# Kernel optimization log

Hardware: AMD Instinct MI355X
Metric: run time of the kernel (lower is better)

The kernel has to match this reference:

```python
import jax, jax.numpy as jnp
import numpy as np

EPS = 0.1  # eps added to covariance sums, as in torch cov()
N, D, N_CLASSES = 4096, 1024, 64


def setup_inputs() -> dict:
    key = jax.random.key(0)
    k1, k2 = jax.random.split(key)
    inputs = jax.random.normal(k1, (N, D), dtype=jnp.float32)
    targets = jax.random.randint(k2, (N,), 0, N_CLASSES, dtype=jnp.int32)
    return {"inputs": inputs, "targets": targets}


def _masked_sqdiff_sum(M, x):
    # Per-dim sum over masked pairs (i,j) of (x_i - x_j)^2, without
    # materializing the [n, n, d] difference tensor:
    #   sum_ij M_ij (x_id^2 + x_jd^2 - 2 x_id x_jd)
    row = M.sum(axis=1)  # [n]
    col = M.sum(axis=0)  # [n]
    x2 = x * x
    return row @ x2 + col @ x2 - 2.0 * jnp.sum(x * (M @ x), axis=0)  # [d]


def _jeffrey_loss(inputs, targets):
    n = inputs.shape[0]
    same = targets[:, None] == targets[None, :]
    eye = jnp.eye(n, dtype=bool)
    pos_m = (same & ~eye).astype(inputs.dtype)  # positive pairs, i != j
    neg_m = (~same).astype(inputs.dtype)        # negative pairs

    # Covariances are computed on detached diffs in the torch code
    xd = jax.lax.stop_gradient(inputs)
    cnt_pos = pos_m.sum()
    cnt_neg = neg_m.sum()
    sigma1 = (_masked_sqdiff_sum(pos_m, xd) + EPS) / cnt_pos  # [d]
    sigma0 = (_masked_sqdiff_sum(neg_m, xd) + EPS) / cnt_neg  # [d]
    weights = 1.0 / sigma0 - 1.0 / sigma1  # [d], constant w.r.t. grad

    # S[i, j] = sum_d weights_d * (x_i - x_j)_d^2, via gram expansion
    xw = inputs * weights            # [n, d]
    sq = jnp.sum(inputs * xw, axis=1)  # [n], sum_d w_d x_d^2
    S = sq[:, None] + sq[None, :] - 2.0 * inputs @ xw.T  # [n, n]

    # BCEWithLogitsLoss(mean): label 1 on positive pairs (logits a),
    # label 0 on negative pairs (logits b)
    loss_sum = jnp.sum(pos_m * jax.nn.softplus(-S)) + jnp.sum(neg_m * jax.nn.softplus(S))
    return loss_sum / (cnt_pos + cnt_neg)


def reference(inputs, targets):
    return _jeffrey_loss(inputs, targets)
```

## Files before the change

kernel.cpp:

```cpp
#include <hip/hip_runtime.h>
#include <stdint.h>

#define N_ROWS 4096
#define DIM    1024
#define NCLS   64
#define EPSV   0.1f

typedef __attribute__((ext_vector_type(8))) __bf16 bf16x8;
typedef __attribute__((ext_vector_type(4))) float  f32x4;

__device__ __forceinline__ unsigned short f2bf(float f) {
    union { float f; unsigned u; } v; v.f = f;
    unsigned r = v.u + 0x7FFF + ((v.u >> 16) & 1);
    return (unsigned short)(r >> 16);
}

__device__ __forceinline__ void async_cp16(const void* g, void* l) {
    __builtin_amdgcn_global_load_lds((const __attribute__((address_space(1))) void*)g,
                                     (__attribute__((address_space(3))) void*)l,
                                     16, 0, 0);
}

__device__ __forceinline__ float softplus(float x) {
    return fmaxf(x, 0.f) + __logf(1.f + __expf(-fabsf(x)));
}

__global__ __launch_bounds__(128) void k_stats(const float* __restrict__ X,
                                               const int* __restrict__ tgt,
                                               float* __restrict__ csum_p,
                                               float* __restrict__ csq_p) {
    __shared__ float csum[NCLS * 128];
    __shared__ float csq[NCLS * 128];
    __shared__ int   tch[128];
    int tid = threadIdx.x;
    int dg = blockIdx.x >> 5, ch = blockIdx.x & 31;
    int d = dg * 128 + tid;
    for (int c = 0; c < NCLS; c++) { csum[c * 128 + tid] = 0.f; csq[c * 128 + tid] = 0.f; }
    tch[tid] = tgt[ch * 128 + tid];
    __syncthreads();
    const float* xp = X + (size_t)(ch * 128) * DIM + d;
    #pragma unroll 4
    for (int r = 0; r < 128; r++) {
        float x = xp[(size_t)r * DIM];
        int t = tch[r];
        csum[t * 128 + tid] += x;
        csq [t * 128 + tid] += x * x;
    }
    for (int c = 0; c < NCLS; c++) {
        csum_p[(size_t)(ch * NCLS + c) * DIM + d] = csum[c * 128 + tid];
        csq_p [(size_t)(ch * NCLS + c) * DIM + d] = csq [c * 128 + tid];
    }
}

__global__ __launch_bounds__(256) void k_reduce(const float* __restrict__ csum_p,
                                                const float* __restrict__ csq_p,
                                                float* __restrict__ csumR,
                                                float* __restrict__ csqR) {
    int idx = blockIdx.x * 256 + threadIdx.x;
    float s = 0.f, q = 0.f;
    #pragma unroll 8
    for (int ch = 0; ch < 32; ch++) {
        s += csum_p[(size_t)ch * NCLS * DIM + idx];
        q += csq_p [(size_t)ch * NCLS * DIM + idx];
    }
    csumR[idx] = s;
    csqR [idx] = q;
}

__global__ __launch_bounds__(256) void k_weights(const int* __restrict__ tgt,
                                                 const float* __restrict__ csumR,
                                                 const float* __restrict__ csqR,
                                                 float* __restrict__ w,
                                                 float* __restrict__ loss_out) {
    __shared__ int hist[NCLS];
    int tid = threadIdx.x;
    if (tid < NCLS) hist[tid] = 0;
    __syncthreads();
    for (int i = tid; i < N_ROWS; i += 256) atomicAdd(&hist[tgt[i]], 1);
    __syncthreads();
    float cnt_pos, cnt_neg;
    {
        long long sp = 0, ss = 0;
        for (int c = 0; c < NCLS; c++) { long long cc = hist[c]; sp += cc * (cc - 1); ss += cc * cc; }
        cnt_pos = (float)sp;
        cnt_neg = (float)((long long)N_ROWS * N_ROWS - ss);
    }
    int d = blockIdx.x * 256 + tid;
    float A = 0.f, X2 = 0.f, T = 0.f, SS = 0.f;
    #pragma unroll 8
    for (int c = 0; c < NCLS; c++) {
        float s = csumR[c * DIM + d];
        float q = csqR [c * DIM + d];
        A += (float)hist[c] * q; X2 += q; T += s; SS += s * s;
    }
    float posnum = 2.f * (A - SS);
    float negnum = 2.f * ((float)N_ROWS * X2 - A - T * T + SS);
    w[d] = cnt_neg / (negnum + EPSV) - cnt_pos / (posnum + EPSV);
    if (blockIdx.x == 0 && tid == 0) loss_out[0] = 0.0f;
}

__global__ __launch_bounds__(256) void k_prep(const float* __restrict__ X,
                                              const float* __restrict__ w,
                                              unsigned short* __restrict__ Xb,
                                              unsigned short* __restrict__ XWb,
                                              float* __restrict__ sq) {
    int row = blockIdx.x, tid = threadIdx.x;
    const float4* xr = (const float4*)(X + (size_t)row * DIM);
    const float4* wr = (const float4*)w;
    float4 x = xr[tid], ww = wr[tid];
    float4 xw = make_float4(x.x * ww.x, x.y * ww.y, x.z * ww.z, x.w * ww.w);
    float p = x.x * xw.x + x.y * xw.y + x.z * xw.z + x.w * xw.w;
    ushort4 xb, xwb;
    xb.x  = f2bf(x.x);  xb.y  = f2bf(x.y);  xb.z  = f2bf(x.z);  xb.w  = f2bf(x.w);
    xwb.x = f2bf(xw.x); xwb.y = f2bf(xw.y); xwb.z = f2bf(xw.z); xwb.w = f2bf(xw.w);
    ((ushort4*)(Xb  + (size_t)row * DIM))[tid] = xb;
    ((ushort4*)(XWb + (size_t)row * DIM))[tid] = xwb;
    for (int off = 32; off; off >>= 1) p += __shfl_down(p, off, 64);
    __shared__ float red[4];
    int wv = tid >> 6, ln = tid & 63;
    if (ln == 0) red[wv] = p;
    __syncthreads();
    if (tid == 0) sq[row] = red[0] + red[1] + red[2] + red[3];
}

__global__ __launch_bounds__(512) void k_gemm_loss(const unsigned short* __restrict__ Xb,
                                                   const unsigned short* __restrict__ XWb,
                                                   const float* __restrict__ sq,
                                                   const int* __restrict__ tgt,
                                                   float* __restrict__ loss) {
    __shared__ __align__(16) unsigned short As[3][128 * 32];
    __shared__ __align__(16) unsigned short Bs[3][128 * 32];
    __shared__ float sqI[128], sqJ[128];
    __shared__ int   tIs[128], tJs[128];
    __shared__ float red[8];

    int tid = threadIdx.x;
    int wave = tid >> 6, lane = tid & 63;

    int g = blockIdx.x & 7, s = blockIdx.x >> 3;
    int sz0 = g + 1, sz1 = g + 9, sz2 = g + 17, sz3 = g + 25;
    int jt, it;
    if      (s < sz0)             { jt = g;      it = s; }
    else if (s < sz0 + sz1)       { jt = g + 8;  it = s - sz0; }
    else if (s < sz0 + sz1 + sz2) { jt = g + 16; it = s - sz0 - sz1; }
    else if (s < sz0 + sz1 + sz2 + sz3) { jt = g + 24; it = s - sz0 - sz1 - sz2; }
    else return;

    const unsigned short* gp[2];
    unsigned short* lb[2];
    #pragma unroll
    for (int si = 0; si < 2; si++) {
        int gI = wave * 2 + si;
        int R  = gI * 16 + (lane >> 2);
        int q  = (lane & 3) ^ ((R >> 1) & 3);
        int r  = R & 127;
        bool isA = R < 128;
        int grow = (isA ? it : jt) * 128 + r;
        const unsigned short* src = isA ? Xb : XWb;
        gp[si] = src + (size_t)grow * DIM + q * 8;
        lb[si] = (isA ? &As[0][0] : &Bs[0][0]) + (gI & 7) * (16 * 32);
    }

    int lr = lane & 15, kq = lane >> 4;
    int offA[4], offB[2];
    int wrow = (wave >> 2) * 64, wcol = (wave & 3) * 32;
    #pragma unroll
    for (int mi = 0; mi < 4; mi++) {
        int row = wrow + mi * 16 + lr;
        offA[mi] = row * 32 + (kq ^ ((row >> 1) & 3)) * 8;
    }
    #pragma unroll
    for (int nj = 0; nj < 2; nj++) {
        int col = wcol + nj * 16 + lr;
        offB[nj] = col * 32 + (kq ^ ((col >> 1) & 3)) * 8;
    }

    f32x4 acc[4][2];
    #pragma unroll
    for (int i = 0; i < 4; i++)
        #pragma unroll
        for (int j = 0; j < 2; j++) acc[i][j] = (f32x4){0.f, 0.f, 0.f, 0.f};

    #pragma unroll
    for (int si = 0; si < 2; si++) async_cp16(gp[si], lb[si]);
    #pragma unroll
    for (int si = 0; si < 2; si++) async_cp16(gp[si] + 32, lb[si] + 128 * 32);

    int rd = 0;
    for (int kk = 0; kk < 32; kk++) {
        if (kk != 31) asm volatile("s_waitcnt vmcnt(2)" ::: "memory");
        else          asm volatile("s_waitcnt vmcnt(0)" ::: "memory");
        asm volatile("s_barrier" ::: "memory");
        if (kk < 30) {
            int wr = rd ? rd - 1 : 2;
            #pragma unroll
            for (int si = 0; si < 2; si++)
                async_cp16(gp[si] + (kk + 2) * 32, lb[si] + wr * (128 * 32));
        }
        const unsigned short* Ab = As[rd];
        const unsigned short* Bb = Bs[rd];
        bf16x8 av[4], bv[2];
        #pragma unroll
        for (int i = 0; i < 4; i++) av[i] = *(const bf16x8*)(Ab + offA[i]);
        #pragma unroll
        for (int j = 0; j < 2; j++) bv[j] = *(const bf16x8*)(Bb + offB[j]);
        #pragma unroll
        for (int i = 0; i < 4; i++)
            #pragma unroll
            for (int j = 0; j < 2; j++)
                acc[i][j] = __builtin_amdgcn_mfma_f32_16x16x32_bf16(av[i], bv[j], acc[i][j], 0, 0, 0);
        rd = (rd == 2) ? 0 : rd + 1;
    }

    __syncthreads();
    if (tid < 128)      { sqI[tid] = sq[it * 128 + tid]; tIs[tid] = tgt[it * 128 + tid]; }
    else if (tid < 256) { int u = tid - 128; sqJ[u] = sq[jt * 128 + u]; tJs[u] = tgt[jt * 128 + u]; }
    __syncthreads();

    float sum = 0.f;
    bool diagTile = (it == jt);
    #pragma unroll
    for (int j = 0; j < 2; j++) {
        int col = wcol + j * 16 + (lane & 15);
        float sj = sqJ[col]; int tj = tJs[col];
        #pragma unroll
        for (int i = 0; i < 4; i++) {
            int rbase = wrow + i * 16 + (lane >> 4) * 4;
            #pragma unroll
            for (int r = 0; r < 4; r++) {
                int rowp = rbase + r;
                float S = sqI[rowp] + sj - 2.f * acc[i][j][r];
                float v;
                if (tIs[rowp] == tj) v = (diagTile && rowp == col) ? 0.f : softplus(-S);
                else                 v = softplus(S);
                sum += v;
            }
        }
    }
    float scale = (diagTile ? 1.f : 2.f) * (1.f / ((float)N_ROWS * (float)(N_ROWS - 1)));
    sum *= scale;
    for (int off = 32; off; off >>= 1) sum += __shfl_down(sum, off, 64);
    if (lane == 0) red[wave] = sum;
    __syncthreads();
    if (tid == 0) {
        float t = 0.f;
        #pragma unroll
        for (int wv = 0; wv < 8; wv++) t += red[wv];
        atomicAdd(loss, t);
    }
}

extern "C" void kernel_launch(void* const* d_in, const int* in_sizes, int n_in,
                              void* d_out, int out_size, void* d_ws, size_t ws_size,
                              hipStream_t stream) {
    const float* X  = (const float*)d_in[0];
    const int* tgt  = (const int*)d_in[1];
    float* out = (float*)d_out;
    char* ws = (char*)d_ws;
    const size_t MB = 1u << 20;

    float* w        = (float*)ws;
    float* sq       = (float*)(ws + 4096);
    unsigned short* Xb  = (unsigned short*)(ws + 1 * MB);
    unsigned short* XWb = (unsigned short*)(ws + 9 * MB);
    float* csum_p   = (float*)(ws + 17 * MB);
    float* csq_p    = (float*)(ws + 25 * MB);
    float* csumR    = (float*)(ws + 33 * MB);
    float* csqR     = (float*)(ws + 33 * MB + 256 * 1024);

    k_stats   <<<256,  128, 0, stream>>>(X, tgt, csum_p, csq_p);
    k_reduce  <<<256,  256, 0, stream>>>(csum_p, csq_p, csumR, csqR);
    k_weights <<<4,    256, 0, stream>>>(tgt, csumR, csqR, w, out);
    k_prep    <<<4096, 256, 0, stream>>>(X, w, Xb, XWb, sq);
    k_gemm_loss<<<640, 512, 0, stream>>>(Xb, XWb, sq, tgt, out);
}
```

Baseline: 136.2 us.

## Fuse per-class stats into one gather kernel and deepen GEMM pipeline to four stages

Replaces the two-kernel per-class statistics pass with a single kernel. Each block compacts the row indices of its class into shared memory, then accumulates the sum and sum of squares directly, which removes the 16 MB of partial-sum writes and the separate reduction launch. Separately, the GEMM's LDS ring grows from three to four stages so three k-tiles are in flight instead of two. The trade-off is more LDS per block, which may reduce occupancy, and an index-gathered read of X where each row is still read contiguously.

```diff
diff --git a/kernel.cpp b/kernel.cpp
--- a/kernel.cpp
+++ b/kernel.cpp
@@ -25,46 +25,29 @@
     return fmaxf(x, 0.f) + __logf(1.f + __expf(-fabsf(x)));
 }
 
-__global__ __launch_bounds__(128) void k_stats(const float* __restrict__ X,
-                                               const int* __restrict__ tgt,
-                                               float* __restrict__ csum_p,
-                                               float* __restrict__ csq_p) {
-    __shared__ float csum[NCLS * 128];
-    __shared__ float csq[NCLS * 128];
-    __shared__ int   tch[128];
-    int tid = threadIdx.x;
-    int dg = blockIdx.x >> 5, ch = blockIdx.x & 31;
-    int d = dg * 128 + tid;
-    for (int c = 0; c < NCLS; c++) { csum[c * 128 + tid] = 0.f; csq[c * 128 + tid] = 0.f; }
-    tch[tid] = tgt[ch * 128 + tid];
-    __syncthreads();
-    const float* xp = X + (size_t)(ch * 128) * DIM + d;
-    #pragma unroll 4
-    for (int r = 0; r < 128; r++) {
-        float x = xp[(size_t)r * DIM];
-        int t = tch[r];
-        csum[t * 128 + tid] += x;
-        csq [t * 128 + tid] += x * x;
-    }
-    for (int c = 0; c < NCLS; c++) {
-        csum_p[(size_t)(ch * NCLS + c) * DIM + d] = csum[c * 128 + tid];
-        csq_p [(size_t)(ch * NCLS + c) * DIM + d] = csq [c * 128 + tid];
-    }
-}
-
-__global__ __launch_bounds__(256) void k_reduce(const float* __restrict__ csum_p,
-                                                const float* __restrict__ csq_p,
+__global__ __launch_bounds__(256) void k_cstats(const float* __restrict__ X,
+                                                const int* __restrict__ tgt,
                                                 float* __restrict__ csumR,
                                                 float* __restrict__ csqR) {
-    int idx = blockIdx.x * 256 + threadIdx.x;
-    float s = 0.f, q = 0.f;
-    #pragma unroll 8
-    for (int ch = 0; ch < 32; ch++) {
-        s += csum_p[(size_t)ch * NCLS * DIM + idx];
-        q += csq_p [(size_t)ch * NCLS * DIM + idx];
-    }
-    csumR[idx] = s;
-    csqR [idx] = q;
+    __shared__ int rows[N_ROWS];
+    __shared__ int nrows_s;
+    int tid = threadIdx.x;
+    int c = blockIdx.x >> 2, q = blockIdx.x & 3;
+    if (tid == 0) nrows_s = 0;
+    __syncthreads();
+    for (int i = tid; i < N_ROWS; i += 256)
+        if (tgt[i] == c) { int p = atomicAdd(&nrows_s, 1); rows[p] = i; }
+    __syncthreads();
+    int n = nrows_s;
+    int d = q * 256 + tid;
+    float s = 0.f, qq = 0.f;
+    #pragma unroll 4
+    for (int r = 0; r < n; r++) {
+        float x = X[(size_t)rows[r] * DIM + d];
+        s += x; qq += x * x;
+    }
+    csumR[c * DIM + d] = s;
+    csqR [c * DIM + d] = qq;
 }
 
 __global__ __launch_bounds__(256) void k_weights(const int* __restrict__ tgt,
@@ -128,8 +111,8 @@
                                                    const float* __restrict__ sq,
                                                    const int* __restrict__ tgt,
                                                    float* __restrict__ loss) {
-    __shared__ __align__(16) unsigned short As[3][128 * 32];
-    __shared__ __align__(16) unsigned short Bs[3][128 * 32];
+    __shared__ __align__(16) unsigned short As[4][128 * 32];
+    __shared__ __align__(16) unsigned short Bs[4][128 * 32];
     __shared__ float sqI[128], sqJ[128];
     __shared__ int   tIs[128], tJs[128];
     __shared__ float red[8];
@@ -182,21 +165,23 @@
         for (int j = 0; j < 2; j++) acc[i][j] = (f32x4){0.f, 0.f, 0.f, 0.f};
 
     #pragma unroll
-    for (int si = 0; si < 2; si++) async_cp16(gp[si], lb[si]);
-    #pragma unroll
-    for (int si = 0; si < 2; si++) async_cp16(gp[si] + 32, lb[si] + 128 * 32);
-
-    int rd = 0;
+    for (int st = 0; st < 3; st++)
+        #pragma unroll
+        for (int si = 0; si < 2; si++)
+            async_cp16(gp[si] + st * 32, lb[si] + st * (128 * 32));
+
     for (int kk = 0; kk < 32; kk++) {
-        if (kk != 31) asm volatile("s_waitcnt vmcnt(2)" ::: "memory");
-        else          asm volatile("s_waitcnt vmcnt(0)" ::: "memory");
+        if      (kk < 30)  asm volatile("s_waitcnt vmcnt(4)" ::: "memory");
+        else if (kk == 30) asm volatile("s_waitcnt vmcnt(2)" ::: "memory");
+        else               asm volatile("s_waitcnt vmcnt(0)" ::: "memory");
         asm volatile("s_barrier" ::: "memory");
-        if (kk < 30) {
-            int wr = rd ? rd - 1 : 2;
+        if (kk < 29) {
+            int wr = (kk + 3) & 3;
             #pragma unroll
             for (int si = 0; si < 2; si++)
-                async_cp16(gp[si] + (kk + 2) * 32, lb[si] + wr * (128 * 32));
+                async_cp16(gp[si] + (kk + 3) * 32, lb[si] + wr * (128 * 32));
         }
+        int rd = kk & 3;
         const unsigned short* Ab = As[rd];
         const unsigned short* Bb = Bs[rd];
         bf16x8 av[4], bv[2];
@@ -209,7 +194,6 @@
             #pragma unroll
             for (int j = 0; j < 2; j++)
                 acc[i][j] = __builtin_amdgcn_mfma_f32_16x16x32_bf16(av[i], bv[j], acc[i][j], 0, 0, 0);
-        rd = (rd == 2) ? 0 : rd + 1;
     }
 
     __syncthreads();
@@ -263,13 +247,10 @@
     float* sq       = (float*)(ws + 4096);
     unsigned short* Xb  = (unsigned short*)(ws + 1 * MB);
     unsigned short* XWb = (unsigned short*)(ws + 9 * MB);
-    float* csum_p   = (float*)(ws + 17 * MB);
-    float* csq_p    = (float*)(ws + 25 * MB);
-    float* csumR    = (float*)(ws + 33 * MB);
-    float* csqR     = (float*)(ws + 33 * MB + 256 * 1024);
-
-    k_stats   <<<256,  128, 0, stream>>>(X, tgt, csum_p, csq_p);
-    k_reduce  <<<256,  256, 0, stream>>>(csum_p, csq_p, csumR, csqR);
+    float* csumR    = (float*)(ws + 17 * MB);
+    float* csqR     = (float*)(ws + 17 * MB + 256 * 1024);
+
+    k_cstats  <<<256,  256, 0, stream>>>(X, tgt, csumR, csqR);
     k_weights <<<4,    256, 0, stream>>>(tgt, csumR, csqR, w, out);
     k_prep    <<<4096, 256, 0, stream>>>(X, w, Xb, XWb, sq);
     k_gemm_loss<<<640, 512, 0, stream>>>(Xb, XWb, sq, tgt, out);
```

New measurement: 127.9 us. 6.1% less time.
